# Kernel tuning notes

Measured on AMD Instinct MI355X. Metric: run time of the kernel, lower is better.

Reference implementation:

```python
import jax, jax.numpy as jnp
import numpy as np

B = 16384
IN = 1024
H = 1024
LN_EPS = 1e-5


def setup_inputs() -> dict:
    key = jax.random.key(0)
    ks = jax.random.split(key, 8)
    # Five gate Linears fused into one weight [IN+H, 5H] (order: f, i, o, c, m)
    scale = 1.0 / np.sqrt(IN + H)
    W = jax.random.uniform(ks[0], (IN + H, 5 * H), jnp.float32, -scale, scale)
    b = jax.random.uniform(ks[1], (5 * H,), jnp.float32, -scale, scale)
    return {
        "x": jax.random.normal(ks[2], (B, IN), jnp.float32),
        "h_prev": jax.random.normal(ks[3], (B, H), jnp.float32),
        "c_prev": jax.random.normal(ks[4], (B, H), jnp.float32),
        "W": W,
        "b": b,
        "ln_gamma": jnp.ones((H,), jnp.float32),
        "ln_beta": jnp.zeros((H,), jnp.float32),
        "retention": jnp.full((H,), 0.9, jnp.float32),
    }


def _layernorm(z, gamma, beta):
    mu = jnp.mean(z, axis=-1, keepdims=True)
    var = jnp.var(z, axis=-1, keepdims=True)
    return (z - mu) * jax.lax.rsqrt(var + LN_EPS) * gamma + beta


def reference(x, h_prev, c_prev, W, b, ln_gamma, ln_beta, retention):
    combined = jnp.concatenate([x, h_prev], axis=-1)        # [B, IN+H]
    gates = combined @ W + b                                # [B, 5H] fused GEMM
    f_pre, i_pre, o_pre, c_pre_act, m_pre = jnp.split(gates, 5, axis=-1)
    f_gate = jax.nn.sigmoid(f_pre)
    i_gate = jax.nn.sigmoid(i_pre)
    o_gate = jax.nn.sigmoid(o_pre)
    c_cand = jnp.tanh(c_pre_act)
    m_gate = jax.nn.sigmoid(m_pre)
    c_new = f_gate * c_prev + i_gate * c_cand
    c_new = c_new * retention + (1.0 - retention) * c_prev
    c_new = m_gate * c_new + (1.0 - m_gate) * c_prev
    # exp(ln)/(1+exp(ln)) == sigmoid(layernorm(o_gate))
    o_exp = jax.nn.sigmoid(_layernorm(o_gate, ln_gamma, ln_beta))
    h_new = o_exp * jnp.tanh(c_new)
    return h_new, c_new
```

## Files before the change

### kernel.cpp

```cpp
#include <hip/hip_runtime.h>
#include <math.h>


typedef unsigned short u16;
typedef unsigned int   u32;
typedef short  short8 __attribute__((ext_vector_type(8)));
typedef float  f32x4  __attribute__((ext_vector_type(4)));
typedef u16    u16x4  __attribute__((ext_vector_type(4)));
typedef u32    u32x4  __attribute__((ext_vector_type(4)));

#define B_ROWS 16384
#define K_DIM  2048
#define N_DIM  5120
#define H_DIM  1024

__device__ __forceinline__ float b2f(u16 u) {
    u32 v = ((u32)u) << 16;
    return __uint_as_float(v);
}
__device__ __forceinline__ u16 f2b(float f) {
    u32 x = __float_as_uint(f);
    u32 r = (x + 0x7fffu + ((x >> 16) & 1u)) >> 16;
    return (u16)r;
}
__device__ __forceinline__ float sigm(float v) {
    return 1.f / (1.f + __expf(-v));
}
__device__ __forceinline__ float tanh_fast(float v) {
    v = fminf(fmaxf(v, -15.f), 15.f);
    float e = __expf(-2.f * v);
    return (1.f - e) / (1.f + e);
}

__global__ __launch_bounds__(256) void convert_A(const float* __restrict__ x,
                                                 const float* __restrict__ h,
                                                 u16* __restrict__ A) {
    size_t idx = ((size_t)blockIdx.x * 256 + threadIdx.x) * 8;
    int row = (int)(idx >> 11);
    int col = (int)(idx & 2047);
    int srcCol = (col & ~63) | (((((col >> 3) & 7) ^ (row & 7))) << 3);
    const float* src = (srcCol < 1024) ? (x + (size_t)row * 1024 + srcCol)
                                       : (h + (size_t)row * 1024 + (srcCol - 1024));
    f32x4 v0 = *(const f32x4*)src;
    f32x4 v1 = *(const f32x4*)(src + 4);
    u32x4 w;
    w.x = (u32)f2b(v0.x) | ((u32)f2b(v0.y) << 16);
    w.y = (u32)f2b(v0.z) | ((u32)f2b(v0.w) << 16);
    w.z = (u32)f2b(v1.x) | ((u32)f2b(v1.y) << 16);
    w.w = (u32)f2b(v1.z) | ((u32)f2b(v1.w) << 16);
    *(u32x4*)(A + idx) = w;
}

__global__ __launch_bounds__(256) void convert_W(const float* __restrict__ W,
                                                 u16* __restrict__ Wt) {
    __shared__ float tile[64][33];
    const int t  = threadIdx.x;
    const int tx = t & 31;
    const int ty = t >> 5;
    const int n0 = blockIdx.x * 32;
    const int k0 = blockIdx.y * 64;
#pragma unroll
    for (int i = 0; i < 8; ++i)
        tile[ty + 8 * i][tx] = W[(size_t)(k0 + ty + 8 * i) * N_DIM + n0 + tx];
    __syncthreads();
    const int n = t >> 3;
    const int s = t & 7;
    const int g = s ^ (n & 7);
    u32x4 w;
    w.x = (u32)f2b(tile[g * 8 + 0][n]) | ((u32)f2b(tile[g * 8 + 1][n]) << 16);
    w.y = (u32)f2b(tile[g * 8 + 2][n]) | ((u32)f2b(tile[g * 8 + 3][n]) << 16);
    w.z = (u32)f2b(tile[g * 8 + 4][n]) | ((u32)f2b(tile[g * 8 + 5][n]) << 16);
    w.w = (u32)f2b(tile[g * 8 + 6][n]) | ((u32)f2b(tile[g * 8 + 7][n]) << 16);
    *(u32x4*)(Wt + (size_t)(n0 + n) * K_DIM + k0 + s * 8) = w;
}

#define BK 64

__device__ __forceinline__ void gld_lds16(const void* g, void* l) {
    __builtin_amdgcn_global_load_lds(
        (const __attribute__((address_space(1))) void*)g,
        (__attribute__((address_space(3))) void*)l, 16, 0, 0);
}

__global__ __launch_bounds__(256) void gemm_gates(const u16* __restrict__ A,
                                                  const u16* __restrict__ Bt,
                                                  const float* __restrict__ bias,
                                                  u16* __restrict__ gates) {
    __shared__ u16 As[128 * BK];
    __shared__ u16 Bs[128 * BK];

    const int t = threadIdx.x;
    const int bid = blockIdx.x;
    const int xcd = bid & 7;
    const int c   = bid >> 3;
    const int m0 = ((xcd << 4) | (c & 15)) << 7;
    const int n0 = (c >> 4) << 7;

    const int l   = t & 63;
    const int wid = t >> 6;
    const int wm  = (wid >> 1) << 6;
    const int wn  = (wid & 1) << 6;
    const int lr  = l & 15;
    const int lh  = l >> 4;
    const int z   = lr & 7;
    const int sA0 = (lh ^ z) * 8;

    const int tb = t >> 3;
    const u16* aPtr = A  + (size_t)(m0 + tb) * K_DIM + (t & 7) * 8;
    const u16* bPtr = Bt + (size_t)(n0 + tb) * K_DIM + (t & 7) * 8;
    const int dOff = t * 8;

    f32x4 acc[4][4] = {};

#pragma unroll 1
    for (int kt = 0; kt < 32; ++kt) {
#pragma unroll
        for (int i = 0; i < 4; ++i) {
            gld_lds16(aPtr + (size_t)(i * 32) * K_DIM, &As[i * 2048 + dOff]);
            gld_lds16(bPtr + (size_t)(i * 32) * K_DIM, &Bs[i * 2048 + dOff]);
        }
        __syncthreads();

        short8 af[4][2], bf[4][2];
#pragma unroll
        for (int m = 0; m < 4; ++m) {
            const int u = (wm + m * 16 + lr) * 64;
            af[m][0] = *(const short8*)&As[u + sA0];
            af[m][1] = *(const short8*)&As[u + (sA0 ^ 32)];
        }
#pragma unroll
        for (int n = 0; n < 4; ++n) {
            const int u = (wn + n * 16 + lr) * 64;
            bf[n][0] = *(const short8*)&Bs[u + sA0];
            bf[n][1] = *(const short8*)&Bs[u + (sA0 ^ 32)];
        }
#pragma unroll
        for (int sk = 0; sk < 2; ++sk)
#pragma unroll
            for (int m = 0; m < 4; ++m)
#pragma unroll
                for (int n = 0; n < 4; ++n)
                    acc[m][n] = __builtin_amdgcn_mfma_f32_16x16x32_bf16(
                        af[m][sk], bf[n][sk], acc[m][n], 0, 0, 0);
        __syncthreads();
        aPtr += BK;
        bPtr += BK;
    }

    const int grp = n0 >> 10;
#pragma unroll
    for (int ni = 0; ni < 4; ++ni) {
        int col = n0 + wn + ni * 16 + lr;
        float bv = bias[col];
#pragma unroll
        for (int mi = 0; mi < 4; ++mi) {
#pragma unroll
            for (int j = 0; j < 4; ++j) {
                int row = m0 + wm + mi * 16 + lh * 4 + j;
                float v = acc[mi][ni][j] + bv;
                float g = (grp == 3) ? tanh_fast(v) : sigm(v);
                gates[(size_t)row * N_DIM + col] = f2b(g);
            }
        }
    }
}

__global__ __launch_bounds__(256) void fuse_out(const u16* __restrict__ gates,
                                                const float* __restrict__ c_prev,
                                                const float* __restrict__ ret,
                                                const float* __restrict__ gamma,
                                                const float* __restrict__ beta,
                                                float* __restrict__ out) {
    const int r = blockIdx.x;
    const int t = threadIdx.x;
    const u16* g = gates + (size_t)r * N_DIM;
    const int j0 = t * 4;

    u16x4 ov = *(const u16x4*)(g + 2048 + j0);
    float o0 = b2f(ov.x), o1 = b2f(ov.y), o2 = b2f(ov.z), o3 = b2f(ov.w);
    float s1 = o0 + o1 + o2 + o3;
    float s2 = o0 * o0 + o1 * o1 + o2 * o2 + o3 * o3;
#pragma unroll
    for (int off = 32; off; off >>= 1) {
        s1 += __shfl_xor(s1, off, 64);
        s2 += __shfl_xor(s2, off, 64);
    }
    __shared__ float red[8];
    if ((t & 63) == 0) { red[t >> 6] = s1; red[4 + (t >> 6)] = s2; }
    __syncthreads();
    float S1 = red[0] + red[1] + red[2] + red[3];
    float S2 = red[4] + red[5] + red[6] + red[7];
    float mu   = S1 * (1.f / 1024.f);
    float var  = S2 * (1.f / 1024.f) - mu * mu;
    float rstd = rsqrtf(var + 1e-5f);

    u16x4 fv = *(const u16x4*)(g + j0);
    u16x4 iv = *(const u16x4*)(g + 1024 + j0);
    u16x4 cv = *(const u16x4*)(g + 3072 + j0);
    u16x4 mv = *(const u16x4*)(g + 4096 + j0);
    f32x4 cp = *(const f32x4*)(c_prev + (size_t)r * H_DIM + j0);
    f32x4 rt = *(const f32x4*)(ret + j0);
    f32x4 gm = *(const f32x4*)(gamma + j0);
    f32x4 bt = *(const f32x4*)(beta + j0);

    float of[4] = {o0, o1, o2, o3};
    u16 fa[4] = {fv.x, fv.y, fv.z, fv.w};
    u16 ia[4] = {iv.x, iv.y, iv.z, iv.w};
    u16 ca[4] = {cv.x, cv.y, cv.z, cv.w};
    u16 ma[4] = {mv.x, mv.y, mv.z, mv.w};

    f32x4 hout, cout;
#pragma unroll
    for (int i = 0; i < 4; ++i) {
        float f = b2f(fa[i]), ig = b2f(ia[i]), cc = b2f(ca[i]), m = b2f(ma[i]);
        float cpv = cp[i], rv = rt[i];
        float c1 = f * cpv + ig * cc;
        float c2 = c1 * rv + (1.f - rv) * cpv;
        float cn = m * c2 + (1.f - m) * cpv;
        float ln = (of[i] - mu) * rstd * gm[i] + bt[i];
        float oe = sigm(ln);
        float hn = oe * tanh_fast(cn);
        hout[i] = hn;
        cout[i] = cn;
    }
    *(f32x4*)(out + (size_t)r * H_DIM + j0) = hout;
    *(f32x4*)(out + (size_t)B_ROWS * H_DIM + (size_t)r * H_DIM + j0) = cout;
}

extern "C" void kernel_launch(void* const* d_in, const int* in_sizes, int n_in,
                              void* d_out, int out_size, void* d_ws, size_t ws_size,
                              hipStream_t stream) {
    const float* x      = (const float*)d_in[0];
    const float* h_prev = (const float*)d_in[1];
    const float* c_prev = (const float*)d_in[2];
    const float* W      = (const float*)d_in[3];
    const float* bias   = (const float*)d_in[4];
    const float* gamma  = (const float*)d_in[5];
    const float* beta   = (const float*)d_in[6];
    const float* ret    = (const float*)d_in[7];
    float* out = (float*)d_out;

    u16* Abuf  = (u16*)d_ws;
    u16* Wt    = Abuf + (size_t)B_ROWS * K_DIM;
    u16* gates = Wt + (size_t)N_DIM * K_DIM;

    convert_A<<<(B_ROWS * K_DIM / 8) / 256, 256, 0, stream>>>(x, h_prev, Abuf);
    convert_W<<<dim3(N_DIM / 32, K_DIM / 64), 256, 0, stream>>>(W, Wt);
    gemm_gates<<<(B_ROWS / 128) * (N_DIM / 128), 256, 0, stream>>>(Abuf, Wt, bias, gates);
    fuse_out<<<B_ROWS, 256, 0, stream>>>(gates, c_prev, ret, gamma, beta, out);
}
```

Before: 517.7 us.

## Pre-fragment A for direct register loads and use 256x256 tiles with multi-buffered B

convert_A now writes A in MFMA-fragment order, so the GEMM loads A operands straight from global memory into registers and skips the LDS staging step. The GEMM tile grows to 256x256 with 512 threads, each wave holding 8x4 accumulators. B is staged through a 4-deep LDS ring with a prefetch distance of 2 and one barrier per k-step. The aim is more operand reuse, less LDS traffic and better overlap of loads with MFMA, at the cost of higher register pressure and reliance on hand-placed waitcnt counts.

```diff
diff --git a/kernel.cpp b/kernel.cpp
--- a/kernel.cpp
+++ b/kernel.cpp
@@ -35,12 +35,16 @@
 __global__ __launch_bounds__(256) void convert_A(const float* __restrict__ x,
                                                  const float* __restrict__ h,
                                                  u16* __restrict__ A) {
-    size_t idx = ((size_t)blockIdx.x * 256 + threadIdx.x) * 8;
-    int row = (int)(idx >> 11);
-    int col = (int)(idx & 2047);
-    int srcCol = (col & ~63) | (((((col >> 3) & 7) ^ (row & 7))) << 3);
-    const float* src = (srcCol < 1024) ? (x + (size_t)row * 1024 + srcCol)
-                                       : (h + (size_t)row * 1024 + (srcCol - 1024));
+    size_t T = (size_t)blockIdx.x * 256 + threadIdx.x;
+    int l  = (int)T & 63;
+    size_t b = T >> 6;
+    int sk = (int)b & 1;
+    int kt = (int)(b >> 1) & 31;
+    int mi = (int)(b >> 6);
+    int row = mi * 16 + (l & 15);
+    int col = kt * 64 + sk * 32 + (l >> 4) * 8;
+    const float* src = (col < 1024) ? (x + (size_t)row * 1024 + col)
+                                    : (h + (size_t)row * 1024 + (col - 1024));
     f32x4 v0 = *(const f32x4*)src;
     f32x4 v1 = *(const f32x4*)(src + 4);
     u32x4 w;
@@ -48,7 +52,7 @@
     w.y = (u32)f2b(v0.z) | ((u32)f2b(v0.w) << 16);
     w.z = (u32)f2b(v1.x) | ((u32)f2b(v1.y) << 16);
     w.w = (u32)f2b(v1.z) | ((u32)f2b(v1.w) << 16);
-    *(u32x4*)(A + idx) = w;
+    *(u32x4*)(A + T * 8) = w;
 }
 
 __global__ __launch_bounds__(256) void convert_W(const float* __restrict__ W,
@@ -82,84 +86,110 @@
         (__attribute__((address_space(3))) void*)l, 16, 0, 0);
 }
 
-__global__ __launch_bounds__(256) void gemm_gates(const u16* __restrict__ A,
-                                                  const u16* __restrict__ Bt,
-                                                  const float* __restrict__ bias,
-                                                  u16* __restrict__ gates) {
-    __shared__ u16 As[128 * BK];
-    __shared__ u16 Bs[128 * BK];
+__global__ __launch_bounds__(512, 2) void gemm_gates(const u16* __restrict__ Af,
+                                                     const u16* __restrict__ Bt,
+                                                     const float* __restrict__ bias,
+                                                     u16* __restrict__ gates) {
+    __shared__ u16 Bs[4][16384];
 
     const int t = threadIdx.x;
     const int bid = blockIdx.x;
     const int xcd = bid & 7;
     const int c   = bid >> 3;
-    const int m0 = ((xcd << 4) | (c & 15)) << 7;
-    const int n0 = (c >> 4) << 7;
+    const int m0 = ((xcd << 3) | (c & 7)) << 8;
+    const int n0 = (c >> 3) << 8;
 
     const int l   = t & 63;
     const int wid = t >> 6;
-    const int wm  = (wid >> 1) << 6;
-    const int wn  = (wid & 1) << 6;
+    const int wr  = wid >> 2;
+    const int wc  = wid & 3;
     const int lr  = l & 15;
     const int lh  = l >> 4;
     const int z   = lr & 7;
     const int sA0 = (lh ^ z) * 8;
 
-    const int tb = t >> 3;
-    const u16* aPtr = A  + (size_t)(m0 + tb) * K_DIM + (t & 7) * 8;
-    const u16* bPtr = Bt + (size_t)(n0 + tb) * K_DIM + (t & 7) * 8;
+    const u16* bPtr = Bt + (size_t)(n0 + (t >> 3)) * K_DIM + (t & 7) * 8;
     const int dOff = t * 8;
 
-    f32x4 acc[4][4] = {};
+    const int MI0 = (m0 >> 4) + wr * 8;
+    const u16* aPtr = Af + (size_t)MI0 * 32768 + l * 8;
+
+    f32x4 acc[8][4] = {};
+    short8 af0[4][2], af1[4][2], bf[4][2];
+
+#define STAGE_B(buf, OFF) do {                                                \
+    _Pragma("unroll") for (int i = 0; i < 4; ++i)                             \
+        gld_lds16(bPtr + (size_t)(i * 64) * K_DIM + (OFF),                    \
+                  &Bs[buf][i * 4096 + dOff]);                                 \
+} while (0)
+
+#define LOAD_AF(dst, QOFF, KOFF) do {                                         \
+    _Pragma("unroll") for (int m = 0; m < 4; ++m)                             \
+    _Pragma("unroll") for (int sk = 0; sk < 2; ++sk)                          \
+        dst[m][sk] = *(const short8*)(aPtr + (QOFF) + (size_t)m * 32768 +     \
+                                      (KOFF) + sk * 512);                     \
+} while (0)
+
+#define MFMA32(AF, q) do {                                                    \
+    _Pragma("unroll") for (int sk = 0; sk < 2; ++sk)                          \
+    _Pragma("unroll") for (int m = 0; m < 4; ++m)                             \
+    _Pragma("unroll") for (int n = 0; n < 4; ++n)                             \
+        acc[(q) * 4 + m][n] = __builtin_amdgcn_mfma_f32_16x16x32_bf16(        \
+            AF[m][sk], bf[n][sk], acc[(q) * 4 + m][n], 0, 0, 0);              \
+} while (0)
+
+    STAGE_B(0, 0);
+    STAGE_B(1, BK);
+    LOAD_AF(af0, 0, 0);
+    LOAD_AF(af1, 131072, 0);
+    asm volatile("s_waitcnt vmcnt(16)" ::: "memory");
+    __builtin_amdgcn_s_barrier();
+    __builtin_amdgcn_sched_barrier(0);
 
 #pragma unroll 1
     for (int kt = 0; kt < 32; ++kt) {
-#pragma unroll
-        for (int i = 0; i < 4; ++i) {
-            gld_lds16(aPtr + (size_t)(i * 32) * K_DIM, &As[i * 2048 + dOff]);
-            gld_lds16(bPtr + (size_t)(i * 32) * K_DIM, &Bs[i * 2048 + dOff]);
+        STAGE_B((kt + 2) & 3, (kt + 2) * BK);
+
+        const u16* B_ = Bs[kt & 3];
+#pragma unroll
+        for (int n = 0; n < 4; ++n) {
+            const int u = (wc * 64 + n * 16 + lr) * 64;
+            bf[n][0] = *(const short8*)&B_[u + sA0];
+            bf[n][1] = *(const short8*)&B_[u + (sA0 ^ 32)];
         }
-        __syncthreads();
-
-        short8 af[4][2], bf[4][2];
-#pragma unroll
-        for (int m = 0; m < 4; ++m) {
-            const int u = (wm + m * 16 + lr) * 64;
-            af[m][0] = *(const short8*)&As[u + sA0];
-            af[m][1] = *(const short8*)&As[u + (sA0 ^ 32)];
-        }
-#pragma unroll
-        for (int n = 0; n < 4; ++n) {
-            const int u = (wn + n * 16 + lr) * 64;
-            bf[n][0] = *(const short8*)&Bs[u + sA0];
-            bf[n][1] = *(const short8*)&Bs[u + (sA0 ^ 32)];
-        }
-#pragma unroll
-        for (int sk = 0; sk < 2; ++sk)
-#pragma unroll
-            for (int m = 0; m < 4; ++m)
-#pragma unroll
-                for (int n = 0; n < 4; ++n)
-                    acc[m][n] = __builtin_amdgcn_mfma_f32_16x16x32_bf16(
-                        af[m][sk], bf[n][sk], acc[m][n], 0, 0, 0);
-        __syncthreads();
-        aPtr += BK;
-        bPtr += BK;
-    }
+
+        MFMA32(af0, 0);
+        LOAD_AF(af0, 0, 1024);
+        MFMA32(af1, 1);
+        LOAD_AF(af1, 131072, 1024);
+
+        aPtr += 1024;
+        asm volatile("s_waitcnt lgkmcnt(0)" ::: "memory");
+        __builtin_amdgcn_s_barrier();
+        __builtin_amdgcn_sched_barrier(0);
+    }
+#undef STAGE_B
+#undef LOAD_AF
+#undef MFMA32
+
+    asm volatile("s_waitcnt vmcnt(0)" ::: "memory");
 
     const int grp = n0 >> 10;
 #pragma unroll
     for (int ni = 0; ni < 4; ++ni) {
-        int col = n0 + wn + ni * 16 + lr;
+        int col = n0 + wc * 64 + ni * 16 + lr;
         float bv = bias[col];
 #pragma unroll
-        for (int mi = 0; mi < 4; ++mi) {
-#pragma unroll
-            for (int j = 0; j < 4; ++j) {
-                int row = m0 + wm + mi * 16 + lh * 4 + j;
-                float v = acc[mi][ni][j] + bv;
-                float g = (grp == 3) ? tanh_fast(v) : sigm(v);
-                gates[(size_t)row * N_DIM + col] = f2b(g);
+        for (int q = 0; q < 2; ++q) {
+#pragma unroll
+            for (int m = 0; m < 4; ++m) {
+#pragma unroll
+                for (int j = 0; j < 4; ++j) {
+                    int row = m0 + wr * 128 + q * 64 + m * 16 + lh * 4 + j;
+                    float v = acc[q * 4 + m][ni][j] + bv;
+                    float g = (grp == 3) ? tanh_fast(v) : sigm(v);
+                    gates[(size_t)row * N_DIM + col] = f2b(g);
+                }
             }
         }
     }
@@ -246,6 +276,6 @@
 
     convert_A<<<(B_ROWS * K_DIM / 8) / 256, 256, 0, stream>>>(x, h_prev, Abuf);
     convert_W<<<dim3(N_DIM / 32, K_DIM / 64), 256, 0, stream>>>(W, Wt);
-    gemm_gates<<<(B_ROWS / 128) * (N_DIM / 128), 256, 0, stream>>>(Abuf, Wt, bias, gates);
+    gemm_gates<<<(B_ROWS / 256) * (N_DIM / 256), 512, 0, stream>>>(Abuf, Wt, bias, gates);
     fuse_out<<<B_ROWS, 256, 0, stream>>>(gates, c_prev, ret, gamma, beta, out);
 }
```

Measured after the change: 520.4 us. Within noise of the previous version (+0.5%).

## Triple-buffer LDS GEMM pipeline with 256x128 tiles and 512-thread blocks

Applied to the files above, without the earlier changes.

Restructures the bf16 gate GEMM into a three-stage LDS ring. Global-to-LDS loads for future k-tiles are issued while MFMAs run on register fragments that were prefetched from the previous stage. Each block grows to 256x128 with 8 waves, and MFMA sections raise wave priority. The aim is to hide global memory latency and remove the two full syncthreads per k-step, at the cost of about 144KB of LDS and one block per CU.

```diff
diff --git a/kernel.cpp b/kernel.cpp
--- a/kernel.cpp
+++ b/kernel.cpp
@@ -82,87 +82,120 @@
         (__attribute__((address_space(3))) void*)l, 16, 0, 0);
 }
 
-__global__ __launch_bounds__(256) void gemm_gates(const u16* __restrict__ A,
-                                                  const u16* __restrict__ Bt,
-                                                  const float* __restrict__ bias,
-                                                  u16* __restrict__ gates) {
-    __shared__ u16 As[128 * BK];
-    __shared__ u16 Bs[128 * BK];
+__global__ __launch_bounds__(512, 1) void gemm_gates(const u16* __restrict__ A,
+                                                     const u16* __restrict__ Bt,
+                                                     const float* __restrict__ bias,
+                                                     u16* __restrict__ gates) {
+    __shared__ u16 lds[3][24576];
 
     const int t = threadIdx.x;
     const int bid = blockIdx.x;
     const int xcd = bid & 7;
     const int c   = bid >> 3;
-    const int m0 = ((xcd << 4) | (c & 15)) << 7;
-    const int n0 = (c >> 4) << 7;
+    const int m0 = ((xcd << 3) | (c & 7)) << 8;
+    const int n0 = (c >> 3) << 7;
 
     const int l   = t & 63;
     const int wid = t >> 6;
-    const int wm  = (wid >> 1) << 6;
-    const int wn  = (wid & 1) << 6;
+    const int wr  = wid >> 1;
+    const int wc  = wid & 1;
     const int lr  = l & 15;
     const int lh  = l >> 4;
     const int z   = lr & 7;
     const int sA0 = (lh ^ z) * 8;
 
-    const int tb = t >> 3;
-    const u16* aPtr = A  + (size_t)(m0 + tb) * K_DIM + (t & 7) * 8;
-    const u16* bPtr = Bt + (size_t)(n0 + tb) * K_DIM + (t & 7) * 8;
+    const u16* aBase = A  + (size_t)(m0 + (t >> 3)) * K_DIM + (t & 7) * 8;
+    const u16* bBase = Bt + (size_t)(n0 + (t >> 3)) * K_DIM + (t & 7) * 8;
     const int dOff = t * 8;
 
     f32x4 acc[4][4] = {};
+    short8 af[2][4][2], bf[2][4][2];
+    u16* p0 = &lds[0][0];
+    u16* p1 = &lds[1][0];
+    u16* p2 = &lds[2][0];
+
+#define STAGE(P, OFF) do {                                                    \
+    _Pragma("unroll") for (int i = 0; i < 4; ++i)                             \
+        gld_lds16(aBase + (size_t)(i * 64) * K_DIM + (OFF),                   \
+                  (P) + i * 4096 + dOff);                                     \
+    _Pragma("unroll") for (int i = 0; i < 2; ++i)                             \
+        gld_lds16(bBase + (size_t)(i * 64) * K_DIM + (OFF),                   \
+                  (P) + 16384 + i * 4096 + dOff);                             \
+} while (0)
+
+#define RD(SET, P) do {                                                       \
+    _Pragma("unroll") for (int m = 0; m < 4; ++m) {                           \
+        const int u_ = (wr * 64 + m * 16 + lr) * 64;                          \
+        af[SET][m][0] = *(const short8*)&(P)[u_ + sA0];                       \
+        af[SET][m][1] = *(const short8*)&(P)[u_ + (sA0 ^ 32)];                \
+    }                                                                         \
+    _Pragma("unroll") for (int n = 0; n < 4; ++n) {                           \
+        const int u_ = 16384 + (wc * 64 + n * 16 + lr) * 64;                  \
+        bf[SET][n][0] = *(const short8*)&(P)[u_ + sA0];                       \
+        bf[SET][n][1] = *(const short8*)&(P)[u_ + (sA0 ^ 32)];                \
+    }                                                                         \
+} while (0)
+
+#define MFMA_T(SET) do {                                                      \
+    __builtin_amdgcn_s_setprio(1);                                            \
+    _Pragma("unroll") for (int sk = 0; sk < 2; ++sk)                          \
+    _Pragma("unroll") for (int m = 0; m < 4; ++m)                             \
+    _Pragma("unroll") for (int n = 0; n < 4; ++n)                             \
+        acc[m][n] = __builtin_amdgcn_mfma_f32_16x16x32_bf16(                  \
+            af[SET][m][sk], bf[SET][n][sk], acc[m][n], 0, 0, 0);              \
+    __builtin_amdgcn_s_setprio(0);                                            \
+} while (0)
+
+#define TILE(CUR, OFF) do {                                                   \
+    STAGE(p0, OFF);                                                           \
+    RD((CUR) ^ 1, p1);                                                        \
+    MFMA_T(CUR);                                                              \
+    asm volatile("s_waitcnt lgkmcnt(0)" ::: "memory");   \
+    asm volatile("s_waitcnt vmcnt(6)" ::: "memory");         \
+    __builtin_amdgcn_s_barrier();                                             \
+    __builtin_amdgcn_sched_barrier(0);                                        \
+    u16* tmp_ = p0; p0 = p1; p1 = p2; p2 = tmp_;             \
+} while (0)
+
+    STAGE(p0, 0); STAGE(p1, 64); STAGE(p2, 128);
+    asm volatile("s_waitcnt vmcnt(6)" ::: "memory");
+    __builtin_amdgcn_s_barrier();
+    __builtin_amdgcn_sched_barrier(0);
+    RD(0, p0);
+    asm volatile("s_waitcnt lgkmcnt(0)" ::: "memory");
+    __builtin_amdgcn_s_barrier();
+    __builtin_amdgcn_sched_barrier(0);
 
 #pragma unroll 1
-    for (int kt = 0; kt < 32; ++kt) {
-#pragma unroll
-        for (int i = 0; i < 4; ++i) {
-            gld_lds16(aPtr + (size_t)(i * 32) * K_DIM, &As[i * 2048 + dOff]);
-            gld_lds16(bPtr + (size_t)(i * 32) * K_DIM, &Bs[i * 2048 + dOff]);
-        }
-        __syncthreads();
-
-        short8 af[4][2], bf[4][2];
+    for (int it = 0; it < 16; ++it) {
+        TILE(0, 192);
+        TILE(1, 256);
+        aBase += 128;
+        bBase += 128;
+    }
+
+    asm volatile("s_waitcnt vmcnt(0)" ::: "memory");
+
+    const int grp = n0 >> 10;
+#pragma unroll
+    for (int ni = 0; ni < 4; ++ni) {
+        int col = n0 + wc * 64 + ni * 16 + lr;
+        float bv = bias[col];
 #pragma unroll
         for (int m = 0; m < 4; ++m) {
-            const int u = (wm + m * 16 + lr) * 64;
-            af[m][0] = *(const short8*)&As[u + sA0];
-            af[m][1] = *(const short8*)&As[u + (sA0 ^ 32)];
-        }
-#pragma unroll
-        for (int n = 0; n < 4; ++n) {
-            const int u = (wn + n * 16 + lr) * 64;
-            bf[n][0] = *(const short8*)&Bs[u + sA0];
-            bf[n][1] = *(const short8*)&Bs[u + (sA0 ^ 32)];
-        }
-#pragma unroll
-        for (int sk = 0; sk < 2; ++sk)
-#pragma unroll
-            for (int m = 0; m < 4; ++m)
-#pragma unroll
-                for (int n = 0; n < 4; ++n)
-                    acc[m][n] = __builtin_amdgcn_mfma_f32_16x16x32_bf16(
-                        af[m][sk], bf[n][sk], acc[m][n], 0, 0, 0);
-        __syncthreads();
-        aPtr += BK;
-        bPtr += BK;
-    }
-
-    const int grp = n0 >> 10;
-#pragma unroll
-    for (int ni = 0; ni < 4; ++ni) {
-        int col = n0 + wn + ni * 16 + lr;
-        float bv = bias[col];
-#pragma unroll
-        for (int mi = 0; mi < 4; ++mi) {
 #pragma unroll
             for (int j = 0; j < 4; ++j) {
-                int row = m0 + wm + mi * 16 + lh * 4 + j;
-                float v = acc[mi][ni][j] + bv;
+                int row = m0 + wr * 64 + m * 16 + lh * 4 + j;
+                float v = acc[m][ni][j] + bv;
                 float g = (grp == 3) ? tanh_fast(v) : sigm(v);
                 gates[(size_t)row * N_DIM + col] = f2b(g);
             }
         }
     }
+#undef STAGE
+#undef RD
+#undef MFMA_T
+#undef TILE
 }
 
 __global__ __launch_bounds__(256) void fuse_out(const u16* __restrict__ gates,
@@ -246,6 +279,6 @@
 
     convert_A<<<(B_ROWS * K_DIM / 8) / 256, 256, 0, stream>>>(x, h_prev, Abuf);
     convert_W<<<dim3(N_DIM / 32, K_DIM / 64), 256, 0, stream>>>(W, Wt);
-    gemm_gates<<<(B_ROWS / 128) * (N_DIM / 128), 256, 0, stream>>>(Abuf, Wt, bias, gates);
+    gemm_gates<<<(B_ROWS / 256) * (N_DIM / 128), 512, 0, stream>>>(Abuf, Wt, bias, gates);
     fuse_out<<<B_ROWS, 256, 0, stream>>>(gates, c_prev, ret, gamma, beta, out);
 }
```

Result: faster. 492.1 us (-4.9%).
